# Optimization experiments

Hardware: AMD Instinct MI355X
Metric: run time of the kernel (lower is better)

## Reference

```python
import jax, jax.numpy as jnp
import numpy as np

N_NODES = 1_000_000
N_EDGES = 16_000_000
NUM_REL = 3
C_IN, C_OUT = 3, 2


def setup_inputs() -> dict:
    key = jax.random.key(0)
    ks = jax.random.split(key, 10)
    x = jax.random.normal(ks[0], (N_NODES, C_IN), dtype=jnp.float32)
    edge_index = jax.random.randint(ks[1], (2, N_EDGES), 0, N_NODES, dtype=jnp.int64)
    edge_attr = jax.random.randint(ks[2], (N_EDGES,), 0, NUM_REL, dtype=jnp.int64)
    s = 0.3
    W1 = jax.random.normal(ks[3], (NUM_REL, C_IN, C_OUT), dtype=jnp.float32) * s
    root1 = jax.random.normal(ks[4], (C_IN, C_OUT), dtype=jnp.float32) * s
    b1 = jax.random.normal(ks[5], (C_OUT,), dtype=jnp.float32) * s
    W2 = jax.random.normal(ks[6], (NUM_REL, C_OUT, C_OUT), dtype=jnp.float32) * s
    root2 = jax.random.normal(ks[7], (C_OUT, C_OUT), dtype=jnp.float32) * s
    b2 = jax.random.normal(ks[8], (C_OUT,), dtype=jnp.float32) * s
    return {"x": x, "edge_index": edge_index, "edge_attr": edge_attr,
            "W1": W1, "root1": root1, "b1": b1,
            "W2": W2, "root2": root2, "b2": b2}


def rgcn_conv(x, edge_index, edge_type, W, root, bias, num_nodes):
    """PyG RGCNConv: per-relation mean-aggregated messages + root transform + bias."""
    src, dst = edge_index[0], edge_index[1]
    xs = x[src]                                    # [E, c_in] gather once
    out = x @ root + bias                          # [N, c_out]
    for r in range(NUM_REL):                       # small fixed relation loop
        mask = (edge_type == r)
        msg = jnp.where(mask[:, None], xs @ W[r], 0.0)          # [E, c_out]
        sums = jax.ops.segment_sum(msg, dst, num_segments=num_nodes)
        cnt = jax.ops.segment_sum(mask.astype(x.dtype), dst, num_segments=num_nodes)
        out = out + sums / jnp.maximum(cnt, 1.0)[:, None]       # mean aggr
    return out


def reference(x, edge_index, edge_attr, W1, root1, b1, W2, root2, b2):
    h = rgcn_conv(x, edge_index, edge_attr, W1, root1, b1, N_NODES)
    h = jax.nn.relu(h)
    # F.dropout(training=self.training): identity in eval mode
    out = rgcn_conv(h, edge_index, edge_attr, W2, root2, b2, N_NODES)
    return out
```

## Files before the change

### kernel.cpp

```cpp
#include <hip/hip_runtime.h>


typedef unsigned long long u64;
typedef unsigned u32;

constexpr int NN = 1000000;
constexpr int NE = 16000000;
constexpr int NR = 3;

constexpr int BSH   = 10;
constexpr int NB    = (NN + 1023) >> 10;
constexpr int BCAP  = 18432;
constexpr int EPB   = 16384;
constexpr int NBLKB = (NE + EPB - 1) / EPB;

__device__ __forceinline__ u32 enc_x(float x0, float x1, float x2) {
    int q0 = __float2int_rn(fminf(fmaxf(x0 * 64.0f, -511.0f), 511.0f));
    int q1 = __float2int_rn(fminf(fmaxf(x1 * 128.0f, -1023.0f), 1023.0f));
    int q2 = __float2int_rn(fminf(fmaxf(x2 * 128.0f, -1023.0f), 1023.0f));
    return ((u32)(q0 + 512) & 0x3FFu)
         | (((u32)(q1 + 1024) & 0x7FFu) << 10)
         | (((u32)(q2 + 1024) & 0x7FFu) << 21);
}

__device__ __forceinline__ u64 widen_x(u32 q) {
    return (u64)(q & 0x3FFu)
         | ((u64)((q >> 10) & 0x7FFu) << 18)
         | ((u64)(q >> 21) << 36)
         | (1ULL << 54);
}

__device__ __forceinline__ u32 enc_h(float h0, float h1) {
    int q0 = __float2int_rn(fminf(h0 * 1024.0f, 32767.0f));
    int q1 = __float2int_rn(fminf(h1 * 1024.0f, 32767.0f));
    return ((u32)q0 & 0xFFFFu) | ((u32)q1 << 16);
}

__device__ __forceinline__ u64 widen_h(u32 q) {
    return (u64)(q & 0xFFFFu)
         | ((u64)(q >> 16) << 22)
         | (1ULL << 44);
}

__device__ __forceinline__ void dec_h(u32 e, float& h0, float& h1) {
    h0 = (float)(e & 0xFFFFu) * (1.0f / 1024.0f);
    h1 = (float)(e >> 16)     * (1.0f / 1024.0f);
}

constexpr u64 M28 = (1ULL << 28) - 1;
__device__ __forceinline__ u64 pack_msg(float m0, float m1) {
    int a0 = __float2int_rn(fmaf(m0, 4096.0f, 524288.0f));
    int a1 = __float2int_rn(fmaf(m1, 4096.0f, 524288.0f));
    return (u64)(u32)a0 | ((u64)(u32)a1 << 28) | (1ULL << 56);
}


__global__ __launch_bounds__(1024, 8) void scatter_kernel(
    const int* __restrict__ src, const int* __restrict__ dst, const int* __restrict__ rel,
    const float* __restrict__ x, u32* __restrict__ qx,
    u32* __restrict__ buf, u32* __restrict__ cursor)
{
    __shared__ u32 stage[EPB];
    __shared__ u32 hist[1024];
    __shared__ u32 wcur[1024];
    __shared__ u32 gbase[1024];
    __shared__ u32 wt[16];
    const int tid = threadIdx.x;
    const int wave = tid >> 6, lane = tid & 63;

    {
        int node = blockIdx.x * 1024 + tid;
        if (node < NN)
            qx[node] = enc_x(x[3 * node + 0], x[3 * node + 1], x[3 * node + 2]);
    }

    hist[tid] = 0;
    __syncthreads();

    const int base = blockIdx.x * EPB;
    const int nloc = min(EPB, NE - base);
    const int g4 = nloc >> 2;
    const int4* dp = (const int4*)(dst + base);
    const int4* sp = (const int4*)(src + base);
    const int4* rp = (const int4*)(rel + base);

    {
        const int i0 = tid, i1 = tid + 1024, i2 = tid + 2048, i3 = tid + 3072;
        const bool v0 = i0 < g4, v1 = i1 < g4, v2 = i2 < g4, v3 = i3 < g4;
        int4 a0, a1, a2, a3;
        if (v0) a0 = dp[i0];
        if (v1) a1 = dp[i1];
        if (v2) a2 = dp[i2];
        if (v3) a3 = dp[i3];
        if (v0) {
            atomicAdd(&hist[((u32)a0.x) >> BSH], 1u);
            atomicAdd(&hist[((u32)a0.y) >> BSH], 1u);
            atomicAdd(&hist[((u32)a0.z) >> BSH], 1u);
            atomicAdd(&hist[((u32)a0.w) >> BSH], 1u);
        }
        if (v1) {
            atomicAdd(&hist[((u32)a1.x) >> BSH], 1u);
            atomicAdd(&hist[((u32)a1.y) >> BSH], 1u);
            atomicAdd(&hist[((u32)a1.z) >> BSH], 1u);
            atomicAdd(&hist[((u32)a1.w) >> BSH], 1u);
        }
        if (v2) {
            atomicAdd(&hist[((u32)a2.x) >> BSH], 1u);
            atomicAdd(&hist[((u32)a2.y) >> BSH], 1u);
            atomicAdd(&hist[((u32)a2.z) >> BSH], 1u);
            atomicAdd(&hist[((u32)a2.w) >> BSH], 1u);
        }
        if (v3) {
            atomicAdd(&hist[((u32)a3.x) >> BSH], 1u);
            atomicAdd(&hist[((u32)a3.y) >> BSH], 1u);
            atomicAdd(&hist[((u32)a3.z) >> BSH], 1u);
            atomicAdd(&hist[((u32)a3.w) >> BSH], 1u);
        }
    }
    __syncthreads();

    {
        int h0 = hist[tid];
        int v0 = h0;
#pragma unroll
        for (int d = 1; d < 64; d <<= 1) {
            int t = __shfl_up(v0, d);
            if (lane >= d) v0 += t;
        }
        if (lane == 63) wt[wave] = (u32)v0;
        __syncthreads();
        u32 off = 0;
#pragma unroll
        for (int wv = 0; wv < 16; ++wv) off += (wv < wave) ? wt[wv] : 0u;
        wcur[tid] = off + (u32)(v0 - h0);
    }
    __syncthreads();

    if (tid < NB) {
        u32 c = hist[tid];
        gbase[tid] = c ? atomicAdd(&cursor[tid], c) : 0u;
    }
    __syncthreads();

    for (int i = tid; i < g4; i += 2048) {
        const int j = i + 1024;
        const bool vj = j < g4;
        int4 d0 = dp[i], s0 = sp[i], r0 = rp[i];
        int4 d1, s1, r1;
        if (vj) { d1 = dp[j]; s1 = sp[j]; r1 = rp[j]; }
        {
            u32 dd = (u32)d0.x, bk = dd >> BSH;
            u32 sl = atomicAdd(&wcur[bk], 1u);
            stage[sl] = (u32)s0.x | ((u32)r0.x << 20) | ((dd & 1023u) << 22);
        }
        {
            u32 dd = (u32)d0.y, bk = dd >> BSH;
            u32 sl = atomicAdd(&wcur[bk], 1u);
            stage[sl] = (u32)s0.y | ((u32)r0.y << 20) | ((dd & 1023u) << 22);
        }
        {
            u32 dd = (u32)d0.z, bk = dd >> BSH;
            u32 sl = atomicAdd(&wcur[bk], 1u);
            stage[sl] = (u32)s0.z | ((u32)r0.z << 20) | ((dd & 1023u) << 22);
        }
        {
            u32 dd = (u32)d0.w, bk = dd >> BSH;
            u32 sl = atomicAdd(&wcur[bk], 1u);
            stage[sl] = (u32)s0.w | ((u32)r0.w << 20) | ((dd & 1023u) << 22);
        }
        if (vj) {
            {
                u32 dd = (u32)d1.x, bk = dd >> BSH;
                u32 sl = atomicAdd(&wcur[bk], 1u);
                stage[sl] = (u32)s1.x | ((u32)r1.x << 20) | ((dd & 1023u) << 22);
            }
            {
                u32 dd = (u32)d1.y, bk = dd >> BSH;
                u32 sl = atomicAdd(&wcur[bk], 1u);
                stage[sl] = (u32)s1.y | ((u32)r1.y << 20) | ((dd & 1023u) << 22);
            }
            {
                u32 dd = (u32)d1.z, bk = dd >> BSH;
                u32 sl = atomicAdd(&wcur[bk], 1u);
                stage[sl] = (u32)s1.z | ((u32)r1.z << 20) | ((dd & 1023u) << 22);
            }
            {
                u32 dd = (u32)d1.w, bk = dd >> BSH;
                u32 sl = atomicAdd(&wcur[bk], 1u);
                stage[sl] = (u32)s1.w | ((u32)r1.w << 20) | ((dd & 1023u) << 22);
            }
        }
    }
    __syncthreads();

    {
        const int sub = lane >> 4;
        const int l16 = lane & 15;
        for (int b = (wave << 2) + sub; b < NB; b += 64) {
            u32 cnt = hist[b];
            if (!cnt) continue;
            u32 ls = wcur[b] - cnt;
            u32 gb = gbase[b];
            u32* bb = buf + (size_t)b * BCAP;
            for (u32 j = l16; j < cnt; j += 16) {
                u32 slot = gb + j;
                if (slot < (u32)BCAP) bb[slot] = stage[ls + j];
            }
        }
    }
}

__global__ __launch_bounds__(512) void agg1_kernel(
    const u32* __restrict__ buf, const u32* __restrict__ cursor,
    const u32* __restrict__ qx, const float* __restrict__ x,
    const float* __restrict__ W1,
    const float* __restrict__ root1, const float* __restrict__ b1,
    u32* __restrict__ qh)
{
    __shared__ u64 acc[1024 * NR];
    __shared__ float w[NR * 3 * 2];
    const int tid = threadIdx.x;
    for (int i = tid; i < 1024 * NR; i += 512) acc[i] = 0;
    if (tid < NR * 3 * 2) w[tid] = W1[tid];
    __syncthreads();

    const int bk = blockIdx.x;
    const int n = min((int)cursor[bk], BCAP);
    const u32* bb = buf + (size_t)bk * BCAP;
    const int n16 = n >> 4;

    for (int g = tid; g < n16; g += 512) {
        const uint4* p = (const uint4*)(bb + ((size_t)g << 4));
        uint4 E0 = p[0], E1 = p[1], E2 = p[2], E3 = p[3];
        u32 e[16] = {E0.x, E0.y, E0.z, E0.w, E1.x, E1.y, E1.z, E1.w,
                     E2.x, E2.y, E2.z, E2.w, E3.x, E3.y, E3.z, E3.w};
        u32 q[16];
#pragma unroll
        for (int j = 0; j < 16; ++j) q[j] = qx[e[j] & 0xFFFFFu];
#pragma unroll
        for (int j = 0; j < 16; ++j)
            atomicAdd(&acc[(e[j] >> 22) * NR + ((e[j] >> 20) & 3u)], widen_x(q[j]));
    }
    for (int i = (n16 << 4) + tid; i < n; i += 512) {
        u32 e0 = bb[i];
        u32 q0 = qx[e0 & 0xFFFFFu];
        atomicAdd(&acc[(e0 >> 22) * NR + ((e0 >> 20) & 3u)], widen_x(q0));
    }
    __syncthreads();

    for (int l = tid; l < 1024; l += 512) {
        int node = (bk << BSH) + l;
        if (node >= NN) continue;
        float x0 = x[3 * node + 0], x1 = x[3 * node + 1], x2 = x[3 * node + 2];
        float o0 = x0 * root1[0] + x1 * root1[2] + x2 * root1[4] + b1[0];
        float o1 = x0 * root1[1] + x1 * root1[3] + x2 * root1[5] + b1[1];
#pragma unroll
        for (int r = 0; r < NR; ++r) {
            u64 wv = acc[l * NR + r];
            u32 c = (u32)(wv >> 54);
            if (c) {
                float inv = 1.0f / (float)c;
                float S0 = (float)(u32)(wv & 0x3FFFFu);
                float S1 = (float)(u32)((wv >> 18) & 0x3FFFFu);
                float S2 = (float)(u32)((wv >> 36) & 0x3FFFFu);
                float m0 = fmaf(S0, inv, -512.0f)  * (1.0f / 64.0f);
                float m1 = fmaf(S1, inv, -1024.0f) * (1.0f / 128.0f);
                float m2 = fmaf(S2, inv, -1024.0f) * (1.0f / 128.0f);
                const float* wr = &w[r * 6];
                o0 += m0 * wr[0] + m1 * wr[2] + m2 * wr[4];
                o1 += m0 * wr[1] + m1 * wr[3] + m2 * wr[5];
            }
        }
        qh[node] = enc_h(fmaxf(o0, 0.0f), fmaxf(o1, 0.0f));
    }
}

__global__ __launch_bounds__(512) void agg2_kernel(
    const u32* __restrict__ buf, const u32* __restrict__ cursor,
    const u32* __restrict__ qh, const float* __restrict__ W2,
    const float* __restrict__ root2, const float* __restrict__ b2,
    float* __restrict__ out)
{
    __shared__ u64 acc[1024 * NR];
    __shared__ float w[NR * 2 * 2];
    const int tid = threadIdx.x;
    for (int i = tid; i < 1024 * NR; i += 512) acc[i] = 0;
    if (tid < NR * 2 * 2) w[tid] = W2[tid];
    __syncthreads();

    const int bk = blockIdx.x;
    const int n = min((int)cursor[bk], BCAP);
    const u32* bb = buf + (size_t)bk * BCAP;
    const int n16 = n >> 4;

    for (int g = tid; g < n16; g += 512) {
        const uint4* p = (const uint4*)(bb + ((size_t)g << 4));
        uint4 E0 = p[0], E1 = p[1], E2 = p[2], E3 = p[3];
        u32 e[16] = {E0.x, E0.y, E0.z, E0.w, E1.x, E1.y, E1.z, E1.w,
                     E2.x, E2.y, E2.z, E2.w, E3.x, E3.y, E3.z, E3.w};
        u32 q[16];
#pragma unroll
        for (int j = 0; j < 16; ++j) q[j] = qh[e[j] & 0xFFFFFu];
#pragma unroll
        for (int j = 0; j < 16; ++j)
            atomicAdd(&acc[(e[j] >> 22) * NR + ((e[j] >> 20) & 3u)], widen_h(q[j]));
    }
    for (int i = (n16 << 4) + tid; i < n; i += 512) {
        u32 e0 = bb[i];
        u32 q0 = qh[e0 & 0xFFFFFu];
        atomicAdd(&acc[(e0 >> 22) * NR + ((e0 >> 20) & 3u)], widen_h(q0));
    }
    __syncthreads();

    for (int l = tid; l < 1024; l += 512) {
        int node = (bk << BSH) + l;
        if (node >= NN) continue;
        float hv0, hv1;
        dec_h(qh[node], hv0, hv1);
        float o0 = hv0 * root2[0] + hv1 * root2[2] + b2[0];
        float o1 = hv0 * root2[1] + hv1 * root2[3] + b2[1];
#pragma unroll
        for (int r = 0; r < NR; ++r) {
            u64 wv = acc[l * NR + r];
            u32 c = (u32)(wv >> 44);
            if (c) {
                float inv = 1.0f / (float)c;
                float m0 = (float)(u32)(wv & 0x3FFFFFu)         * inv * (1.0f / 1024.0f);
                float m1 = (float)(u32)((wv >> 22) & 0x3FFFFFu) * inv * (1.0f / 1024.0f);
                const float* wr = &w[r * 4];
                o0 += m0 * wr[0] + m1 * wr[2];
                o1 += m0 * wr[1] + m1 * wr[3];
            }
        }
        float2 ov; ov.x = o0; ov.y = o1;
        ((float2*)out)[node] = ov;
    }
}


__global__ __launch_bounds__(256) void edge1_kernel(
    const int* __restrict__ src, const int* __restrict__ dst, const int* __restrict__ rel,
    const float* __restrict__ x, const float* __restrict__ W1,
    u64* __restrict__ sums1)
{
    __shared__ float w[NR * 3 * 2];
    if (threadIdx.x < NR * 3 * 2) w[threadIdx.x] = W1[threadIdx.x];
    __syncthreads();
    int e = blockIdx.x * 256 + threadIdx.x;
    if (e >= NE) return;
    int s = src[e], d = dst[e], r = rel[e];
    float x0 = x[3 * s + 0], x1 = x[3 * s + 1], x2 = x[3 * s + 2];
    const float* wr = &w[r * 6];
    float m0 = x0 * wr[0] + x1 * wr[2] + x2 * wr[4];
    float m1 = x0 * wr[1] + x1 * wr[3] + x2 * wr[5];
    atomicAdd(&sums1[d * NR + r], pack_msg(m0, m1));
}

__global__ __launch_bounds__(256) void node1_kernel(
    const float* __restrict__ x, const u64* __restrict__ sums1,
    const float* __restrict__ root1, const float* __restrict__ b1,
    float* __restrict__ h)
{
    int n = blockIdx.x * 256 + threadIdx.x;
    if (n >= NN) return;
    float x0 = x[3 * n + 0], x1 = x[3 * n + 1], x2 = x[3 * n + 2];
    float o0 = x0 * root1[0] + x1 * root1[2] + x2 * root1[4] + b1[0];
    float o1 = x0 * root1[1] + x1 * root1[3] + x2 * root1[5] + b1[1];
#pragma unroll
    for (int r = 0; r < NR; ++r) {
        u64 wv = sums1[n * NR + r];
        int c = (int)(wv >> 56);
        int s0i = (int)(wv & M28) - (c << 19);
        int s1i = (int)((wv >> 28) & M28) - (c << 19);
        float inv = (1.0f / 4096.0f) / (float)(c > 1 ? c : 1);
        o0 += (float)s0i * inv;
        o1 += (float)s1i * inv;
    }
    float2 hv;
    hv.x = fmaxf(o0, 0.0f);
    hv.y = fmaxf(o1, 0.0f);
    ((float2*)h)[n] = hv;
}

__global__ __launch_bounds__(256) void edge2_kernel(
    const int* __restrict__ src, const int* __restrict__ dst, const int* __restrict__ rel,
    const float* __restrict__ h, const float* __restrict__ W2,
    u64* __restrict__ sums2)
{
    __shared__ float w[NR * 2 * 2];
    if (threadIdx.x < NR * 2 * 2) w[threadIdx.x] = W2[threadIdx.x];
    __syncthreads();
    int e = blockIdx.x * 256 + threadIdx.x;
    if (e >= NE) return;
    int s = src[e];
    float2 hs = ((const float2*)h)[s];
    if (hs.x == 0.0f && hs.y == 0.0f) return;
    int d = dst[e], r = rel[e];
    const float* wr = &w[r * 4];
    float m0 = hs.x * wr[0] + hs.y * wr[2];
    float m1 = hs.x * wr[1] + hs.y * wr[3];
    atomicAdd(&sums2[d * NR + r], pack_msg(m0, m1));
}

__global__ __launch_bounds__(256) void node2_kernel(
    const float* __restrict__ h, const u64* __restrict__ sums1, const u64* __restrict__ sums2,
    const float* __restrict__ root2, const float* __restrict__ b2,
    float* __restrict__ out)
{
    int n = blockIdx.x * 256 + threadIdx.x;
    if (n >= NN) return;
    float2 hv = ((const float2*)h)[n];
    float o0 = hv.x * root2[0] + hv.y * root2[2] + b2[0];
    float o1 = hv.x * root2[1] + hv.y * root2[3] + b2[1];
#pragma unroll
    for (int r = 0; r < NR; ++r) {
        u64 w1 = sums1[n * NR + r];
        u64 w2 = sums2[n * NR + r];
        int c    = (int)(w1 >> 56);
        int adds = (int)(w2 >> 56);
        int s0i = (int)(w2 & M28) - (adds << 19);
        int s1i = (int)((w2 >> 28) & M28) - (adds << 19);
        float inv = (1.0f / 4096.0f) / (float)(c > 1 ? c : 1);
        o0 += (float)s0i * inv;
        o1 += (float)s1i * inv;
    }
    float2 ov; ov.x = o0; ov.y = o1;
    ((float2*)out)[n] = ov;
}

extern "C" void kernel_launch(void* const* d_in, const int* in_sizes, int n_in,
                              void* d_out, int out_size, void* d_ws, size_t ws_size,
                              hipStream_t stream) {
    const float* x     = (const float*)d_in[0];
    const int*   ei    = (const int*)d_in[1];
    const int*   rel   = (const int*)d_in[2];
    const float* W1    = (const float*)d_in[3];
    const float* root1 = (const float*)d_in[4];
    const float* b1    = (const float*)d_in[5];
    const float* W2    = (const float*)d_in[6];
    const float* root2 = (const float*)d_in[7];
    const float* b2    = (const float*)d_in[8];
    float* out = (float*)d_out;

    const int* src = ei;
    const int* dst = ei + NE;

    char* ws = (char*)d_ws;
    const int nb = (NN + 255) / 256;

    const size_t OFF_QX  = 72024064;
    const size_t OFF_QH  = 76024064;
    const size_t OFF_CUR = 80024064;
    const size_t WS_NEED = OFF_CUR + (size_t)NB * sizeof(u32);

    if (ws_size >= WS_NEED) {
        u32* buf    = (u32*)ws;
        u32* qx     = (u32*)(ws + OFF_QX);
        u32* qh     = (u32*)(ws + OFF_QH);
        u32* cursor = (u32*)(ws + OFF_CUR);

        hipMemsetAsync(cursor, 0, (size_t)NB * sizeof(u32), stream);
        scatter_kernel<<<NBLKB, 1024, 0, stream>>>(src, dst, rel, x, qx, buf, cursor);
        agg1_kernel<<<NB, 512, 0, stream>>>(buf, cursor, qx, x, W1, root1, b1, qh);
        agg2_kernel<<<NB, 512, 0, stream>>>(buf, cursor, qh, W2, root2, b2, out);
    } else {
        u64*   sums1 = (u64*)ws;
        u64*   sums2 = (u64*)(ws + (size_t)24 * 1000 * 1000);
        float* h     = (float*)(ws + (size_t)48 * 1000 * 1000);
        const int eb = (NE + 255) / 256;

        hipMemsetAsync(sums1, 0, (size_t)NN * NR * sizeof(u64), stream);
        hipMemsetAsync(sums2, 0, (size_t)NN * NR * sizeof(u64), stream);
        edge1_kernel<<<eb, 256, 0, stream>>>(src, dst, rel, x, W1, sums1);
        node1_kernel<<<nb, 256, 0, stream>>>(x, sums1, root1, b1, h);
        edge2_kernel<<<eb, 256, 0, stream>>>(src, dst, rel, h, W2, sums2);
        node2_kernel<<<nb, 256, 0, stream>>>(h, sums1, sums2, root2, b2, out);
    }
}
```

Before: 460.8 us.

## Scatter edges directly to global buckets, dropping local sort and prefix scan

```diff
diff --git a/kernel.cpp b/kernel.cpp
--- a/kernel.cpp
+++ b/kernel.cpp
@@ -63,10 +63,7 @@
     __shared__ u32 stage[EPB];
     __shared__ u32 hist[1024];
     __shared__ u32 wcur[1024];
-    __shared__ u32 gbase[1024];
-    __shared__ u32 wt[16];
     const int tid = threadIdx.x;
-    const int wave = tid >> 6, lane = tid & 63;
 
     {
         int node = blockIdx.x * 1024 + tid;
@@ -86,31 +83,31 @@
 
     {
         const int i0 = tid, i1 = tid + 1024, i2 = tid + 2048, i3 = tid + 3072;
-        const bool v0 = i0 < g4, v1 = i1 < g4, v2 = i2 < g4, v3 = i3 < g4;
-        int4 a0, a1, a2, a3;
-        if (v0) a0 = dp[i0];
-        if (v1) a1 = dp[i1];
+        const bool v2 = i2 < g4, v3 = i3 < g4;
+        int4 a0 = dp[i0];
+        int4 a1 = dp[i1];
+        int4 a2, a3;
         if (v2) a2 = dp[i2];
         if (v3) a3 = dp[i3];
-        if (v0) {
-            atomicAdd(&hist[((u32)a0.x) >> BSH], 1u);
-            atomicAdd(&hist[((u32)a0.y) >> BSH], 1u);
-            atomicAdd(&hist[((u32)a0.z) >> BSH], 1u);
-            atomicAdd(&hist[((u32)a0.w) >> BSH], 1u);
-        }
-        if (v1) {
-            atomicAdd(&hist[((u32)a1.x) >> BSH], 1u);
-            atomicAdd(&hist[((u32)a1.y) >> BSH], 1u);
-            atomicAdd(&hist[((u32)a1.z) >> BSH], 1u);
-            atomicAdd(&hist[((u32)a1.w) >> BSH], 1u);
-        }
+        ((int4*)stage)[i0] = a0;
+        atomicAdd(&hist[((u32)a0.x) >> BSH], 1u);
+        atomicAdd(&hist[((u32)a0.y) >> BSH], 1u);
+        atomicAdd(&hist[((u32)a0.z) >> BSH], 1u);
+        atomicAdd(&hist[((u32)a0.w) >> BSH], 1u);
+        ((int4*)stage)[i1] = a1;
+        atomicAdd(&hist[((u32)a1.x) >> BSH], 1u);
+        atomicAdd(&hist[((u32)a1.y) >> BSH], 1u);
+        atomicAdd(&hist[((u32)a1.z) >> BSH], 1u);
+        atomicAdd(&hist[((u32)a1.w) >> BSH], 1u);
         if (v2) {
+            ((int4*)stage)[i2] = a2;
             atomicAdd(&hist[((u32)a2.x) >> BSH], 1u);
             atomicAdd(&hist[((u32)a2.y) >> BSH], 1u);
             atomicAdd(&hist[((u32)a2.z) >> BSH], 1u);
             atomicAdd(&hist[((u32)a2.w) >> BSH], 1u);
         }
         if (v3) {
+            ((int4*)stage)[i3] = a3;
             atomicAdd(&hist[((u32)a3.x) >> BSH], 1u);
             atomicAdd(&hist[((u32)a3.y) >> BSH], 1u);
             atomicAdd(&hist[((u32)a3.z) >> BSH], 1u);
@@ -119,93 +116,46 @@
     }
     __syncthreads();
 
-    {
-        int h0 = hist[tid];
-        int v0 = h0;
-#pragma unroll
-        for (int d = 1; d < 64; d <<= 1) {
-            int t = __shfl_up(v0, d);
-            if (lane >= d) v0 += t;
-        }
-        if (lane == 63) wt[wave] = (u32)v0;
-        __syncthreads();
-        u32 off = 0;
-#pragma unroll
-        for (int wv = 0; wv < 16; ++wv) off += (wv < wave) ? wt[wv] : 0u;
-        wcur[tid] = off + (u32)(v0 - h0);
-    }
-    __syncthreads();
-
     if (tid < NB) {
         u32 c = hist[tid];
-        gbase[tid] = c ? atomicAdd(&cursor[tid], c) : 0u;
-    }
-    __syncthreads();
-
-    for (int i = tid; i < g4; i += 2048) {
-        const int j = i + 1024;
-        const bool vj = j < g4;
-        int4 d0 = dp[i], s0 = sp[i], r0 = rp[i];
-        int4 d1, s1, r1;
-        if (vj) { d1 = dp[j]; s1 = sp[j]; r1 = rp[j]; }
+        wcur[tid] = c ? atomicAdd(&cursor[tid], c) : 0u;
+    }
+    __syncthreads();
+
+#pragma unroll
+    for (int k = 0; k < 4; ++k) {
+        const int i = tid + (k << 10);
+        if (k >= 2 && i >= g4) continue;
+        int4 s = sp[i];
+        int4 r = rp[i];
+        uint4 d = ((const uint4*)stage)[i];
         {
-            u32 dd = (u32)d0.x, bk = dd >> BSH;
+            u32 dd = d.x, bk = dd >> BSH;
             u32 sl = atomicAdd(&wcur[bk], 1u);
-            stage[sl] = (u32)s0.x | ((u32)r0.x << 20) | ((dd & 1023u) << 22);
+            if (sl < (u32)BCAP)
+                buf[(size_t)bk * BCAP + sl] =
+                    (u32)s.x | ((u32)r.x << 20) | ((dd & 1023u) << 22);
         }
         {
-            u32 dd = (u32)d0.y, bk = dd >> BSH;
+            u32 dd = d.y, bk = dd >> BSH;
             u32 sl = atomicAdd(&wcur[bk], 1u);
-            stage[sl] = (u32)s0.y | ((u32)r0.y << 20) | ((dd & 1023u) << 22);
+            if (sl < (u32)BCAP)
+                buf[(size_t)bk * BCAP + sl] =
+                    (u32)s.y | ((u32)r.y << 20) | ((dd & 1023u) << 22);
         }
         {
-            u32 dd = (u32)d0.z, bk = dd >> BSH;
+            u32 dd = d.z, bk = dd >> BSH;
             u32 sl = atomicAdd(&wcur[bk], 1u);
-            stage[sl] = (u32)s0.z | ((u32)r0.z << 20) | ((dd & 1023u) << 22);
+            if (sl < (u32)BCAP)
+                buf[(size_t)bk * BCAP + sl] =
+                    (u32)s.z | ((u32)r.z << 20) | ((dd & 1023u) << 22);
         }
         {
-            u32 dd = (u32)d0.w, bk = dd >> BSH;
+            u32 dd = d.w, bk = dd >> BSH;
             u32 sl = atomicAdd(&wcur[bk], 1u);
-            stage[sl] = (u32)s0.w | ((u32)r0.w << 20) | ((dd & 1023u) << 22);
-        }
-        if (vj) {
-            {
-                u32 dd = (u32)d1.x, bk = dd >> BSH;
-                u32 sl = atomicAdd(&wcur[bk], 1u);
-                stage[sl] = (u32)s1.x | ((u32)r1.x << 20) | ((dd & 1023u) << 22);
-            }
-            {
-                u32 dd = (u32)d1.y, bk = dd >> BSH;
-                u32 sl = atomicAdd(&wcur[bk], 1u);
-                stage[sl] = (u32)s1.y | ((u32)r1.y << 20) | ((dd & 1023u) << 22);
-            }
-            {
-                u32 dd = (u32)d1.z, bk = dd >> BSH;
-                u32 sl = atomicAdd(&wcur[bk], 1u);
-                stage[sl] = (u32)s1.z | ((u32)r1.z << 20) | ((dd & 1023u) << 22);
-            }
-            {
-                u32 dd = (u32)d1.w, bk = dd >> BSH;
-                u32 sl = atomicAdd(&wcur[bk], 1u);
-                stage[sl] = (u32)s1.w | ((u32)r1.w << 20) | ((dd & 1023u) << 22);
-            }
-        }
-    }
-    __syncthreads();
-
-    {
-        const int sub = lane >> 4;
-        const int l16 = lane & 15;
-        for (int b = (wave << 2) + sub; b < NB; b += 64) {
-            u32 cnt = hist[b];
-            if (!cnt) continue;
-            u32 ls = wcur[b] - cnt;
-            u32 gb = gbase[b];
-            u32* bb = buf + (size_t)b * BCAP;
-            for (u32 j = l16; j < cnt; j += 16) {
-                u32 slot = gb + j;
-                if (slot < (u32)BCAP) bb[slot] = stage[ls + j];
-            }
+            if (sl < (u32)BCAP)
+                buf[(size_t)bk * BCAP + sl] =
+                    (u32)s.w | ((u32)r.w << 20) | ((dd & 1023u) << 22);
         }
     }
 }
```

Result: slower. 595.6 us (+29.3%).
